# Performance work log

Hardware: AMD Instinct MI355X
Metric: run time of the kernel (lower is better)

Reference implementation:

```python
import jax, jax.numpy as jnp
import numpy as np

NUM_FEAT = 1024
NUM_GROUP = 16
DIM_K = NUM_FEAT // NUM_GROUP  # 64
FEAT_DIM = 64
WAVE_LENGTH = 1000.0


def position_embedding(box, ctx_box):
    # box: (M,4), ctx_box: (N,4) corner encoding -> (M*N, 64)
    xmin, ymin, xmax, ymax = jnp.split(box, 4, axis=1)            # (M,1) each
    bw = xmax - xmin + 1.0
    bh = ymax - ymin + 1.0
    cx = 0.5 * (xmin + xmax)
    cy = 0.5 * (ymin + ymax)
    cxmin, cymin, cxmax, cymax = jnp.split(ctx_box, 4, axis=1)    # (N,1) each
    cbw = cxmax - cxmin + 1.0
    cbh = cymax - cymin + 1.0
    ccx = 0.5 * (cxmin + cxmax)
    ccy = 0.5 * (cymin + cymax)
    dx = jnp.log(jnp.clip(jnp.abs((cx - ccx.T) / bw), 1e-3))      # (M,N)
    dy = jnp.log(jnp.clip(jnp.abs((cy - ccy.T) / bh), 1e-3))
    dw = jnp.log(cbw.T / bw)
    dh = jnp.log(cbh.T / bh)
    pos = jnp.stack((dx, dy, dw, dh), axis=2)                     # (M,N,4)
    feat_range = jnp.arange(FEAT_DIM // 8, dtype=jnp.float32)     # (8,)
    dim_mat = jnp.power(jnp.float32(WAVE_LENGTH), (8.0 / FEAT_DIM) * feat_range)
    div = (100.0 * pos)[..., None] / dim_mat                      # (M,N,4,8)
    emb = jnp.concatenate((jnp.sin(div), jnp.cos(div)), axis=3)   # (M,N,4,16)
    M, N = pos.shape[0], pos.shape[1]
    return emb.reshape(M * N, FEAT_DIM)


def setup_inputs() -> dict:
    key = jax.random.key(0)
    ks = jax.random.split(key, 12)
    M, N = 512, 1024

    def make_boxes(k, n):
        k1, k2 = jax.random.split(k)
        xy = jax.random.uniform(k1, (n, 2), dtype=jnp.float32) * 800.0
        wh = jax.random.uniform(k2, (n, 2), dtype=jnp.float32) * 200.0 + 1.0
        return jnp.concatenate([xy, xy + wh], axis=1)             # valid corners

    return {
        "feat": jax.random.normal(ks[0], (M, NUM_FEAT), dtype=jnp.float32),
        "ctx_feat": jax.random.normal(ks[1], (N, NUM_FEAT), dtype=jnp.float32),
        "box": make_boxes(ks[2], M),
        "ctx_box": make_boxes(ks[3], N),
        # torch Linear stores weight as (out, in); apply as x @ W.T + b
        "w_fc_gt": jax.random.normal(ks[4], (NUM_FEAT, 1024), dtype=jnp.float32) * 0.01,
        "b_fc_gt": jnp.zeros((NUM_FEAT,), dtype=jnp.float32),
        "w_fc_ctx": jax.random.normal(ks[5], (NUM_FEAT, 1024), dtype=jnp.float32) * 0.01,
        "b_fc_ctx": jnp.zeros((NUM_FEAT,), dtype=jnp.float32),
        "w_pos_gt": jax.random.normal(ks[6], (NUM_GROUP, FEAT_DIM), dtype=jnp.float32) * 0.01,
        "b_pos_gt": jnp.zeros((NUM_GROUP,), dtype=jnp.float32),
        "w_pos_ctx": jax.random.normal(ks[7], (NUM_GROUP, FEAT_DIM), dtype=jnp.float32) * 0.01,
        "b_pos_ctx": jnp.zeros((NUM_GROUP,), dtype=jnp.float32),
        # grouped 1x1 conv (16384 -> 1024, groups=16): per-group weight (64 out, 1024 in)
        "w_conv": jax.random.normal(ks[8], (NUM_GROUP, DIM_K, NUM_FEAT), dtype=jnp.float32) * 0.02,
        "b_conv": jnp.zeros((NUM_FEAT,), dtype=jnp.float32),
    }


def reference(feat, ctx_feat, box, ctx_box,
              w_fc_gt, b_fc_gt, w_fc_ctx, b_fc_ctx,
              w_pos_gt, b_pos_gt, w_pos_ctx, b_pos_ctx,
              w_conv, b_conv):
    M, N = feat.shape[0], ctx_feat.shape[0]
    # positional bias per group: (M*N,64) -relu-> linear -> (G,M,N)
    pe_gt = jax.nn.relu(position_embedding(box, ctx_box))
    pos_gt = (pe_gt @ w_pos_gt.T + b_pos_gt).T.reshape(NUM_GROUP, M, N)
    pe_ctx = jax.nn.relu(position_embedding(ctx_box, box))
    pos_ctx = (pe_ctx @ w_pos_ctx.T + b_pos_ctx).T.reshape(NUM_GROUP, N, M)
    # grouped projections
    q = (feat @ w_fc_gt.T + b_fc_gt).reshape(M, NUM_GROUP, DIM_K)
    k = (ctx_feat @ w_fc_ctx.T + b_fc_ctx).reshape(N, NUM_GROUP, DIM_K)
    scores = jnp.einsum('mgd,ngd->gmn', q, k) / np.float32(np.sqrt(DIM_K))  # (G,M,N)
    # gt <- ctx attention with log-position bias
    w1 = jax.nn.softmax(jnp.log(jnp.clip(pos_gt, 1e-6)) + scores, axis=-1)  # (G,M,N)
    att1 = jnp.einsum('gmn,nc->mgc', w1, ctx_feat)                          # (M,G,1024)
    out_gt = jnp.einsum('mgc,goc->mgo', att1, w_conv).reshape(M, NUM_FEAT) + b_conv
    # ctx <- gt attention (note: original module reuses gt_ctx_linear_out here)
    w2 = jax.nn.softmax(jnp.log(jnp.clip(pos_ctx, 1e-6)) + scores.transpose(0, 2, 1), axis=-1)  # (G,N,M)
    att2 = jnp.einsum('gnm,mc->ngc', w2, feat)                              # (N,G,1024)
    out_ctx = jnp.einsum('ngc,goc->ngo', att2, w_conv).reshape(N, NUM_FEAT) + b_conv
    return out_gt, out_ctx
```

## Files before the change

kernel.cpp:

```cpp
#include <hip/hip_runtime.h>
#include <math.h>


typedef __attribute__((ext_vector_type(8))) short short8;
typedef __attribute__((ext_vector_type(4))) float floatx4;
typedef __attribute__((ext_vector_type(4))) _Float16 half4;
typedef __attribute__((ext_vector_type(4))) unsigned uint4v;

__device__ inline unsigned short f32_bf16_rne(float x) {
    union { float f; unsigned u; } v; v.f = x;
    unsigned u = v.u;
    return (unsigned short)((u + 0x7fffu + ((u >> 16) & 1u)) >> 16);
}

__device__ inline unsigned fbits(float x) {
    union { float f; unsigned u; } v; v.f = x; return v.u;
}
__device__ inline float bitsf(unsigned u) {
    union { unsigned u; float f; } v; v.u = u; return v.f;
}

__device__ __forceinline__ floatx4 mfma16(short8 a, short8 b, floatx4 c) {
    return __builtin_amdgcn_mfma_f32_16x16x32_bf16(a, b, c, 0, 0, 0);
}

__device__ __forceinline__ void gemm_tile_pack(
    const unsigned short* __restrict__ Ab, int lda,
    const unsigned short* __restrict__ Bb, int ldb, int K,
    unsigned short* __restrict__ out_base,
    const float* __restrict__ biasvec,
    unsigned short* As, unsigned short* Bs)
{
    const int tid = threadIdx.x;
    const int lr = tid >> 3;
    const int lk = (tid & 7) * 8;
    const int lane = tid & 63;
    const int wave = tid >> 6;
    const int qr = (wave >> 1) * 32;
    const int qc = (wave & 1) * 32;
    const int m = lane & 15;
    const int quad = lane >> 4;

    const unsigned short* Ap  = Ab + (long long)lr * lda + lk;
    const unsigned short* Ap2 = Ap + 32LL * lda;
    const unsigned short* Bp  = Bb + (long long)lr * ldb + lk;
    const unsigned short* Bp2 = Bp + 32LL * ldb;
    unsigned short* AsW  = As + lr * 72 + lk;
    unsigned short* AsW2 = As + (lr + 32) * 72 + lk;
    unsigned short* BsW  = Bs + lr * 72 + lk;
    unsigned short* BsW2 = Bs + (lr + 32) * 72 + lk;
    const unsigned short* a0p = As + (qr + m) * 72 + quad * 8;
    const unsigned short* b0p = Bs + (qc + m) * 72 + quad * 8;

    floatx4 acc00 = {0.f,0.f,0.f,0.f}, acc01 = {0.f,0.f,0.f,0.f};
    floatx4 acc10 = {0.f,0.f,0.f,0.f}, acc11 = {0.f,0.f,0.f,0.f};

    int4 pa0 = *(const int4*)Ap;
    int4 pa1 = *(const int4*)Ap2;
    int4 pb0 = *(const int4*)Bp;
    int4 pb1 = *(const int4*)Bp2;
    int4 qa0 = *(const int4*)(Ap + 64);
    int4 qa1 = *(const int4*)(Ap2 + 64);
    int4 qb0 = *(const int4*)(Bp + 64);
    int4 qb1 = *(const int4*)(Bp2 + 64);

    for (int k0 = 0; ; ) {
        __syncthreads();
        *(int4*)AsW  = pa0;
        *(int4*)AsW2 = pa1;
        *(int4*)BsW  = pb0;
        *(int4*)BsW2 = pb1;
        __syncthreads();
        pa0 = qa0; pa1 = qa1; pb0 = qb0; pb1 = qb1;
        const int kf = k0 + 128;
        if (kf < K) {
            qa0 = *(const int4*)(Ap + kf);
            qa1 = *(const int4*)(Ap2 + kf);
            qb0 = *(const int4*)(Bp + kf);
            qb1 = *(const int4*)(Bp2 + kf);
        }
        #pragma unroll
        for (int kk = 0; kk < 64; kk += 32) {
            short8 a0 = *(const short8*)(a0p + kk);
            short8 a1 = *(const short8*)(a0p + 16 * 72 + kk);
            short8 b0 = *(const short8*)(b0p + kk);
            short8 b1 = *(const short8*)(b0p + 16 * 72 + kk);
            acc00 = mfma16(a0, b0, acc00);
            acc01 = mfma16(a0, b1, acc01);
            acc10 = mfma16(a1, b0, acc10);
            acc11 = mfma16(a1, b1, acc11);
        }
        k0 += 64;
        if (k0 >= K) break;
    }

    float bias0 = 0.f, bias1 = 0.f;
    if (biasvec) { bias0 = biasvec[qc + m]; bias1 = biasvec[qc + 16 + m]; }

    __syncthreads();
    const floatx4 accs[2][2] = { {acc00, acc01}, {acc10, acc11} };
    #pragma unroll
    for (int i = 0; i < 2; ++i)
        #pragma unroll
        for (int r = 0; r < 4; ++r) {
            const int lrow = qr + i * 16 + quad * 4 + r;
            #pragma unroll
            for (int j = 0; j < 2; ++j) {
                const int lcol = qc + j * 16 + m;
                float val = accs[i][j][r] + (j ? bias1 : bias0);
                As[lrow * 72 + lcol] = f32_bf16_rne(val);
            }
        }
    __syncthreads();
    #pragma unroll
    for (int h = 0; h < 2; ++h) {
        const int f = h * 2048 + tid * 8;
        const int lanep = (f >> 3) & 63;
        const int part = (f >> 9) & 1;
        const int ploc = f >> 10;
        const int row = ploc * 16 + (lanep & 15);
        const int col = part * 32 + ((lanep >> 4) << 3);
        short8 v8 = *(const short8*)&As[row * 72 + col];
        *(short8*)(out_base + f) = v8;
    }
}

__global__ __launch_bounds__(256) void cast_kernel(
    const float* __restrict__ s0, unsigned short* __restrict__ d0,
    const float* __restrict__ s1, unsigned short* __restrict__ d1,
    const float* __restrict__ s2, unsigned short* __restrict__ d2,
    const float* __restrict__ s3, unsigned short* __restrict__ d3,
    const float* __restrict__ s4, unsigned short* __restrict__ d4)
{
    int bc = blockIdx.x;
    const float* s; unsigned short* d;
    if (bc < 512)       { s = s0; d = d0; }
    else if (bc < 1536) { s = s1; d = d1; bc -= 512; }
    else if (bc < 2560) { s = s2; d = d2; bc -= 1536; }
    else if (bc < 3584) { s = s3; d = d3; bc -= 2560; }
    else                { s = s4; d = d4; bc -= 3584; }
    const int idx = (bc * 256 + threadIdx.x) * 4;
    float4 v = *(const float4*)(s + idx);
    ushort4 o;
    o.x = f32_bf16_rne(v.x); o.y = f32_bf16_rne(v.y);
    o.z = f32_bf16_rne(v.z); o.w = f32_bf16_rne(v.w);
    *(ushort4*)(d + idx) = o;
}

__global__ __launch_bounds__(256) void posproj_kernel(
    const float* __restrict__ box, const float* __restrict__ ctx_box,
    const float* __restrict__ w_gt, const float* __restrict__ b_gt,
    const float* __restrict__ w_ctx, const float* __restrict__ b_ctx,
    _Float16* __restrict__ bias_gt, _Float16* __restrict__ bias_ctx,
    const unsigned short* __restrict__ in_bf, const unsigned short* __restrict__ wgt,
    const unsigned short* __restrict__ wctx,
    const float* __restrict__ bgt, const float* __restrict__ bctx,
    unsigned short* __restrict__ qk_pack,
    const unsigned short* __restrict__ wconv, unsigned short* __restrict__ vt_pack)
{
    __shared__ __align__(16) unsigned short smem[64 * 72 * 2];
    const int i = blockIdx.x;

    if (i < 4608 && (i % 6) == 0) {
        const int gi = i / 6;
        const int z = gi / 384;
        const int rem = gi - z * 384;
        const int g = rem / 24;
        const int cc = rem - g * 24;
        unsigned short* As = smem;
        unsigned short* Bs = smem + 64 * 72;
        if (z == 0) {
            const int bm = cc * 64;
            const unsigned short* B = (bm < 512) ? wgt : wctx;
            const float* bias = (bm < 512) ? bgt : bctx;
            gemm_tile_pack(in_bf + (long long)bm * 1024, 1024,
                           B + (long long)g * 65536, 1024, 1024,
                           qk_pack + ((long long)g * 96 + cc * 4) * 1024,
                           bias + g * 64, As, Bs);
        } else {
            gemm_tile_pack(wconv + (long long)g * 65536, 1024,
                           in_bf + (long long)cc * 65536, 1024, 1024,
                           vt_pack + ((long long)g * 24 + cc) * 4096,
                           nullptr, As, Bs);
        }
        return;
    }

    const int pi = (i < 4608) ? (i - i / 6 - 1) : (i - 768);
    const bool first = (pi < 2048);
    const long long blk = first ? pi : (pi - 2048);
    const float* boxA = first ? box : ctx_box;
    const float* boxB = first ? ctx_box : box;
    const float* w_pos = first ? w_gt : w_ctx;
    const float* b_pos = first ? b_gt : b_ctx;
    _Float16* out = first ? bias_gt : bias_ctx;
    const int shift = first ? 10 : 9;

    unsigned short* BsH = smem;
    unsigned short* BsL = smem + 16 * 72;
    float* posL = (float*)(smem + 32 * 72);
    _Float16* stg = (_Float16*)(posL + 4 * 68);

    const int tid = threadIdx.x;

    {
        const int g = tid >> 4;
        const int d = (tid & 15) * 4;
        float4 wv = *(const float4*)(w_pos + g * 64 + d);
        unsigned u0 = fbits(wv.x), u1 = fbits(wv.y);
        unsigned u2 = fbits(wv.z), u3 = fbits(wv.w);
        unsigned r0 = fbits(wv.x - bitsf(u0 & 0xFFFF0000u));
        unsigned r1 = fbits(wv.y - bitsf(u1 & 0xFFFF0000u));
        unsigned r2 = fbits(wv.z - bitsf(u2 & 0xFFFF0000u));
        unsigned r3 = fbits(wv.w - bitsf(u3 & 0xFFFF0000u));
        uint2 hv, lv;
        hv.x = (u0 >> 16) | (u1 & 0xFFFF0000u);
        hv.y = (u2 >> 16) | (u3 & 0xFFFF0000u);
        lv.x = (r0 >> 16) | (r1 & 0xFFFF0000u);
        lv.y = (r2 >> 16) | (r3 & 0xFFFF0000u);
        *(uint2*)&BsH[g * 72 + d] = hv;
        *(uint2*)&BsL[g * 72 + d] = lv;
    }
    __syncthreads();

    const int lane = tid & 63;
    const int w = tid >> 6;
    const int m = lane & 15;
    const int quad = lane >> 4;
    const bool qlow = (quad < 2);
    const float phase = (quad & 1) ? 1.57079632679f : 0.0f;
    const float bpv = b_pos[m];

    const unsigned short* bpH = &BsH[m * 72 + quad * 8];
    const unsigned short* bpL = &BsL[m * 72 + quad * 8];
    short8 bH0 = *(const short8*)bpH;
    short8 bH1 = *(const short8*)(bpH + 32);
    short8 bL0 = *(const short8*)bpL;
    short8 bL1 = *(const short8*)(bpL + 32);

    const float w100[8] = {100.f, 42.169650342f, 17.782794100f, 7.498942093f,
                           3.162277660f, 1.333521432f, 0.562341325f, 0.237137371f};
    const long long pbase = blk * 256;

    for (int it = 0; it < 4; ++it) {
        const long long pb = pbase + it * 64;

        {
            const int pl = tid & 63;
            const int p = tid >> 6;
            const long long pair = pb + pl;
            const int i2 = (int)(pair >> shift);
            const int j2 = (int)(pair & ((1 << shift) - 1));
            float4 ba = *(const float4*)(boxA + i2 * 4);
            float4 bb = *(const float4*)(boxB + j2 * 4);
            float posv;
            if (p == 0) {
                float r = __builtin_amdgcn_rcpf(ba.z - ba.x + 1.f);
                posv = __logf(fmaxf(fabsf((0.5f*(ba.x+ba.z) - 0.5f*(bb.x+bb.z)) * r), 1e-3f));
            } else if (p == 1) {
                float r = __builtin_amdgcn_rcpf(ba.w - ba.y + 1.f);
                posv = __logf(fmaxf(fabsf((0.5f*(ba.y+ba.w) - 0.5f*(bb.y+bb.w)) * r), 1e-3f));
            } else if (p == 2) {
                float r = __builtin_amdgcn_rcpf(ba.z - ba.x + 1.f);
                posv = __logf((bb.z - bb.x + 1.f) * r);
            } else {
                float r = __builtin_amdgcn_rcpf(ba.w - ba.y + 1.f);
                posv = __logf((bb.w - bb.y + 1.f) * r);
            }
            posL[p * 68 + pl] = posv;
        }
        __syncthreads();

        const int plB = w * 16 + m;
        const float pos_lo = posL[(qlow ? 0 : 1) * 68 + plB];
        const float pos_hi = posL[(qlow ? 2 : 3) * 68 + plB];

        unsigned hp0[4], lp0[4], hp1[4], lp1[4];
        #pragma unroll
        for (int fi = 0; fi < 4; ++fi) {
            float x0 = fmaxf(__sinf(fmaf(w100[2*fi],     pos_lo, phase)), 0.f);
            float x1 = fmaxf(__sinf(fmaf(w100[2*fi + 1], pos_lo, phase)), 0.f);
            unsigned u0 = fbits(x0), u1 = fbits(x1);
            unsigned r0 = fbits(x0 - bitsf(u0 & 0xFFFF0000u));
            unsigned r1 = fbits(x1 - bitsf(u1 & 0xFFFF0000u));
            hp0[fi] = (u0 >> 16) | (u1 & 0xFFFF0000u);
            lp0[fi] = (r0 >> 16) | (r1 & 0xFFFF0000u);
            float y0 = fmaxf(__sinf(fmaf(w100[2*fi],     pos_hi, phase)), 0.f);
            float y1 = fmaxf(__sinf(fmaf(w100[2*fi + 1], pos_hi, phase)), 0.f);
            unsigned v0 = fbits(y0), v1 = fbits(y1);
            unsigned s0r = fbits(y0 - bitsf(v0 & 0xFFFF0000u));
            unsigned s1r = fbits(y1 - bitsf(v1 & 0xFFFF0000u));
            hp1[fi] = (v0 >> 16) | (v1 & 0xFFFF0000u);
            lp1[fi] = (s0r >> 16) | (s1r & 0xFFFF0000u);
        }
        union { uint4v u; short8 s; } cH0, cL0, cH1, cL1;
        cH0.u = (uint4v){hp0[0], hp0[1], hp0[2], hp0[3]};
        cL0.u = (uint4v){lp0[0], lp0[1], lp0[2], lp0[3]};
        cH1.u = (uint4v){hp1[0], hp1[1], hp1[2], hp1[3]};
        cL1.u = (uint4v){lp1[0], lp1[1], lp1[2], lp1[3]};

        floatx4 acc = {0.f, 0.f, 0.f, 0.f};
        acc = mfma16(cH0.s, bH0, acc);
        acc = mfma16(cH1.s, bH1, acc);
        acc = mfma16(cH0.s, bL0, acc);
        acc = mfma16(cH1.s, bL1, acc);
        acc = mfma16(cL0.s, bH0, acc);
        acc = mfma16(cL1.s, bH1, acc);

        #pragma unroll
        for (int r = 0; r < 4; ++r)
            stg[m * 68 + w * 16 + quad * 4 + r] =
                (_Float16)__logf(fmaxf(acc[r] + bpv, 1e-6f));
        __syncthreads();

        const int g2 = tid >> 4, c16 = tid & 15;
        *(half4*)(out + (long long)g2 * 524288 + pb + c16 * 4) =
            *(const half4*)&stg[g2 * 68 + c16 * 4];
    }
}

template <int NC>
__device__ __forceinline__ void attn_body(
    int g, int bx,
    const unsigned short* __restrict__ qk, int pA, int pB0,
    const _Float16* __restrict__ bias,
    const unsigned short* __restrict__ vt, int cc0,
    const float* __restrict__ b_conv, float* __restrict__ outp,
    unsigned short* wpack, float* redA, float* redB)
{
    constexpr int NCOL = NC * 64;
    constexpr int WS = NCOL + 8;
    constexpr int SHIFT = (NC == 16) ? 10 : 9;

    const int bm = bx * 16;
    const int tid = threadIdx.x;
    const int lane = tid & 63;
    const int w = tid >> 6;
    const int m = lane & 15;
    const int quad = lane >> 4;

    _Float16* bb = (_Float16*)wpack;
    {
        const _Float16* bsrc = bias + (long long)g * 524288 + (long long)bm * NCOL;
        #pragma unroll
        for (int i = 0; i < (16 * NCOL) / (256 * 8); ++i) {
            const int idx = (i * 256 + tid) * 8;
            const int row = idx >> SHIFT;
            const int col = idx & (NCOL - 1);
            *(int4*)(bb + row * WS + col) = *(const int4*)(bsrc + idx);
        }
    }

    const unsigned short* abase = qk + ((long long)(g * 96 + pA)) * 1024;
    short8 aq0 = *(const short8*)(abase + lane * 8);
    short8 aq1 = *(const short8*)(abase + 512 + lane * 8);

    const unsigned short* bptr = qk + ((long long)(g * 96 + pB0 + w)) * 1024 + lane * 8;
    short8 B0[2], B1[2];
    B0[0] = *(const short8*)bptr;
    B1[0] = *(const short8*)(bptr + 512);
    B0[1] = *(const short8*)(bptr + 4096);
    B1[1] = *(const short8*)(bptr + 4096 + 512);

    __syncthreads();

    const _Float16* brow = bb + (quad * 4) * WS + w * 16 + m;

    float v[NC][4];
    #pragma unroll
    for (int c = 0; c < NC; ++c) {
        float bv[4];
        #pragma unroll
        for (int r = 0; r < 4; ++r)
            bv[r] = (float)brow[r * WS + c * 64];
        floatx4 acc = {0.f, 0.f, 0.f, 0.f};
        acc = mfma16(aq0, B0[c & 1], acc);
        acc = mfma16(aq1, B1[c & 1], acc);
        if (c + 2 < NC) {
            const unsigned short* nb = bptr + (long long)(c + 2) * 4096;
            B0[c & 1] = *(const short8*)nb;
            B1[c & 1] = *(const short8*)(nb + 512);
        }
        #pragma unroll
        for (int r = 0; r < 4; ++r)
            v[c][r] = fmaf(0.125f, acc[r], bv[r]);
    }

    const unsigned short* vptr = vt + ((long long)(g * 24 + cc0)) * 4096
                               + w * 1024 + lane * 8;
    short8 V0[2], V1[2];
    V0[0] = *(const short8*)vptr;
    V1[0] = *(const short8*)(vptr + 512);
    V0[1] = *(const short8*)(vptr + 4096);
    V1[1] = *(const short8*)(vptr + 4096 + 512);

    float rmax[4];
    #pragma unroll
    for (int r = 0; r < 4; ++r) {
        float mx = v[0][r];
        #pragma unroll
        for (int c = 1; c < NC; ++c) mx = fmaxf(mx, v[c][r]);
        #pragma unroll
        for (int off = 1; off < 16; off <<= 1)
            mx = fmaxf(mx, __shfl_xor(mx, off, 64));
        rmax[r] = mx;
    }
    if (m == 0) {
        #pragma unroll
        for (int r = 0; r < 4; ++r) redA[w * 16 + quad * 4 + r] = rmax[r];
    }
    __syncthreads();
    #pragma unroll
    for (int r = 0; r < 4; ++r)
        rmax[r] = fmaxf(fmaxf(redA[quad*4+r], redA[16 + quad*4+r]),
                        fmaxf(redA[32 + quad*4+r], redA[48 + quad*4+r]));

    float rsum[4] = {0.f, 0.f, 0.f, 0.f};
    #pragma unroll
    for (int c = 0; c < NC; ++c)
        #pragma unroll
        for (int r = 0; r < 4; ++r) {
            v[c][r] = __expf(v[c][r] - rmax[r]);
            rsum[r] += v[c][r];
        }
    #pragma unroll
    for (int r = 0; r < 4; ++r)
        #pragma unroll
        for (int off = 1; off < 16; off <<= 1)
            rsum[r] += __shfl_xor(rsum[r], off, 64);
    if (m == 0) {
        #pragma unroll
        for (int r = 0; r < 4; ++r) redB[w * 16 + quad * 4 + r] = rsum[r];
    }
    __syncthreads();
    float rinv[4];
    #pragma unroll
    for (int r = 0; r < 4; ++r)
        rinv[r] = 1.f / (redB[quad*4+r] + redB[16 + quad*4+r] +
                         redB[32 + quad*4+r] + redB[48 + quad*4+r]);

    #pragma unroll
    for (int c = 0; c < NC; ++c)
        #pragma unroll
        for (int r = 0; r < 4; ++r)
            wpack[(quad * 4 + r) * WS + c * 64 + w * 16 + m] =
                f32_bf16_rne(v[c][r] * rinv[r]);

    __syncthreads();

    floatx4 oacc = {0.f, 0.f, 0.f, 0.f};
    const unsigned short* awp = wpack + m * WS + quad * 8;
    #pragma unroll
    for (int kc = 0; kc < NC; ++kc) {
        short8 a0 = *(const short8*)(awp + kc * 64);
        short8 a1 = *(const short8*)(awp + kc * 64 + 32);
        oacc = mfma16(a0, V0[kc & 1], oacc);
        oacc = mfma16(a1, V1[kc & 1], oacc);
        if (kc + 2 < NC) {
            const unsigned short* nv = vptr + (long long)(kc + 2) * 4096;
            V0[kc & 1] = *(const short8*)nv;
            V1[kc & 1] = *(const short8*)(nv + 512);
        }
    }

    const int o = w * 16 + m;
    const float bc = b_conv[g * 64 + o];
    __syncthreads();
    float* ot = (float*)wpack;
    #pragma unroll
    for (int r = 0; r < 4; ++r)
        ot[(quad * 4 + r) * 68 + o] = oacc[r] + bc;
    __syncthreads();
    const int orow = tid >> 4, oc4 = (tid & 15) * 4;
    float4 ov = *(const float4*)&ot[orow * 68 + oc4];
    *(float4*)(outp + (long long)(bm + orow) * 1024 + g * 64 + oc4) = ov;
}

__global__ __launch_bounds__(256) void attn_out_kernel(
    const unsigned short* __restrict__ qk_pack,
    const _Float16* __restrict__ bias_gt, const _Float16* __restrict__ bias_ctx,
    const unsigned short* __restrict__ vt_pack, const float* __restrict__ b_conv,
    float* __restrict__ out_gt, float* __restrict__ out_ctx)
{
    __shared__ __align__(16) unsigned short wpack[16 * 1032];
    __shared__ float redA[64], redB[64];

    const int bx = blockIdx.x;
    if (bx < 512) {
        const int rb = bx & 31;
        attn_body<16>(bx >> 5, rb, qk_pack, rb, 32,
                      bias_gt, vt_pack, 8, b_conv, out_gt,
                      wpack, redA, redB);
    } else {
        const int b2 = bx - 512;
        const int rb = b2 & 63;
        attn_body<8>(b2 >> 6, rb, qk_pack, 32 + rb, 0,
                     bias_ctx, vt_pack, 0, b_conv, out_ctx,
                     wpack, redA, redB);
    }
}

extern "C" void kernel_launch(void* const* d_in, const int* in_sizes, int n_in,
                              void* d_out, int out_size, void* d_ws, size_t ws_size,
                              hipStream_t stream)
{
    const float* feat     = (const float*)d_in[0];
    const float* ctx_feat = (const float*)d_in[1];
    const float* box      = (const float*)d_in[2];
    const float* ctx_box  = (const float*)d_in[3];
    const float* w_fc_gt  = (const float*)d_in[4];
    const float* b_fc_gt  = (const float*)d_in[5];
    const float* w_fc_ctx = (const float*)d_in[6];
    const float* b_fc_ctx = (const float*)d_in[7];
    const float* w_pos_gt = (const float*)d_in[8];
    const float* b_pos_gt = (const float*)d_in[9];
    const float* w_pos_ctx= (const float*)d_in[10];
    const float* b_pos_ctx= (const float*)d_in[11];
    const float* w_conv   = (const float*)d_in[12];
    const float* b_conv   = (const float*)d_in[13];

    float* ws = (float*)d_ws;
    unsigned short* in_bf   = (unsigned short*)ws;
    unsigned short* ctx_bf  = in_bf + 524288LL;
    unsigned short* qk_pack = in_bf + 1572864LL;
    _Float16* bias_gt  = (_Float16*)(ws + 1572864LL);
    _Float16* bias_ctx = (_Float16*)(ws + 5767168LL);
    unsigned short* wconv_bf = (unsigned short*)(ws + 9961472LL);
    unsigned short* vt_pack  = (unsigned short*)(ws + 10485760LL);
    unsigned short* wfcgt_bf = (unsigned short*)(ws + 11272192LL);
    unsigned short* wfcctx_bf= wfcgt_bf + 1048576LL;

    float* out_gt  = (float*)d_out;
    float* out_ctx = (float*)d_out + 524288LL;

    hipLaunchKernelGGL(cast_kernel, dim3(4608), dim3(256), 0, stream,
                       feat, in_bf,
                       ctx_feat, ctx_bf,
                       w_fc_gt, wfcgt_bf,
                       w_fc_ctx, wfcctx_bf,
                       w_conv, wconv_bf);

    hipLaunchKernelGGL(posproj_kernel, dim3(4864), dim3(256), 0, stream,
                       box, ctx_box, w_pos_gt, b_pos_gt, w_pos_ctx, b_pos_ctx,
                       bias_gt, bias_ctx,
                       in_bf, wfcgt_bf, wfcctx_bf, b_fc_gt, b_fc_ctx, qk_pack,
                       wconv_bf, vt_pack);

    hipLaunchKernelGGL(attn_out_kernel, dim3(1536), dim3(256), 0, stream,
                       qk_pack, bias_gt, bias_ctx, vt_pack, b_conv, out_gt, out_ctx);
}
```

Before: 150.9 us.

## Load GEMM MFMA operands directly from global memory, bypassing LDS staging

The projection GEMM tile no longer stages A and B tiles through shared memory with two barriers per k-step. Each wave now loads its MFMA operand fragments directly from global memory into registers, prefetching one k-step ahead. Shared memory for the fused kernel is halved, which may help occupancy of the position-projection blocks. The cost is that each operand row is fetched redundantly by several waves, and the per-lane 16-byte global loads are less coalesced, so more traffic goes to the cache.

```diff
diff --git a/kernel.cpp b/kernel.cpp
--- a/kernel.cpp
+++ b/kernel.cpp
@@ -24,16 +24,14 @@
     return __builtin_amdgcn_mfma_f32_16x16x32_bf16(a, b, c, 0, 0, 0);
 }
 
-__device__ __forceinline__ void gemm_tile_pack(
+__device__ __forceinline__ void gemm_tile_pack_direct(
     const unsigned short* __restrict__ Ab, int lda,
     const unsigned short* __restrict__ Bb, int ldb, int K,
     unsigned short* __restrict__ out_base,
     const float* __restrict__ biasvec,
-    unsigned short* As, unsigned short* Bs)
+    unsigned short* As)
 {
     const int tid = threadIdx.x;
-    const int lr = tid >> 3;
-    const int lk = (tid & 7) * 8;
     const int lane = tid & 63;
     const int wave = tid >> 6;
     const int qr = (wave >> 1) * 32;
@@ -41,63 +39,53 @@
     const int m = lane & 15;
     const int quad = lane >> 4;
 
-    const unsigned short* Ap  = Ab + (long long)lr * lda + lk;
-    const unsigned short* Ap2 = Ap + 32LL * lda;
-    const unsigned short* Bp  = Bb + (long long)lr * ldb + lk;
-    const unsigned short* Bp2 = Bp + 32LL * ldb;
-    unsigned short* AsW  = As + lr * 72 + lk;
-    unsigned short* AsW2 = As + (lr + 32) * 72 + lk;
-    unsigned short* BsW  = Bs + lr * 72 + lk;
-    unsigned short* BsW2 = Bs + (lr + 32) * 72 + lk;
-    const unsigned short* a0p = As + (qr + m) * 72 + quad * 8;
-    const unsigned short* b0p = Bs + (qc + m) * 72 + quad * 8;
+    const unsigned short* Arow0 = Ab + (long long)(qr + m) * lda + quad * 8;
+    const unsigned short* Arow1 = Arow0 + 16LL * lda;
+    const unsigned short* Brow0 = Bb + (long long)(qc + m) * ldb + quad * 8;
+    const unsigned short* Brow1 = Brow0 + 16LL * ldb;
 
     floatx4 acc00 = {0.f,0.f,0.f,0.f}, acc01 = {0.f,0.f,0.f,0.f};
     floatx4 acc10 = {0.f,0.f,0.f,0.f}, acc11 = {0.f,0.f,0.f,0.f};
 
-    int4 pa0 = *(const int4*)Ap;
-    int4 pa1 = *(const int4*)Ap2;
-    int4 pb0 = *(const int4*)Bp;
-    int4 pb1 = *(const int4*)Bp2;
-    int4 qa0 = *(const int4*)(Ap + 64);
-    int4 qa1 = *(const int4*)(Ap2 + 64);
-    int4 qb0 = *(const int4*)(Bp + 64);
-    int4 qb1 = *(const int4*)(Bp2 + 64);
+    short8 ca0 = *(const short8*)(Arow0);
+    short8 ca1 = *(const short8*)(Arow1);
+    short8 cb0 = *(const short8*)(Brow0);
+    short8 cb1 = *(const short8*)(Brow1);
+    short8 da0 = *(const short8*)(Arow0 + 32);
+    short8 da1 = *(const short8*)(Arow1 + 32);
+    short8 db0 = *(const short8*)(Brow0 + 32);
+    short8 db1 = *(const short8*)(Brow1 + 32);
 
     for (int k0 = 0; ; ) {
-        __syncthreads();
-        *(int4*)AsW  = pa0;
-        *(int4*)AsW2 = pa1;
-        *(int4*)BsW  = pb0;
-        *(int4*)BsW2 = pb1;
-        __syncthreads();
-        pa0 = qa0; pa1 = qa1; pb0 = qb0; pb1 = qb1;
-        const int kf = k0 + 128;
+        const int kf = k0 + 64;
+        short8 ea0, ea1, eb0, eb1, fa0, fa1, fb0, fb1;
         if (kf < K) {
-            qa0 = *(const int4*)(Ap + kf);
-            qa1 = *(const int4*)(Ap2 + kf);
-            qb0 = *(const int4*)(Bp + kf);
-            qb1 = *(const int4*)(Bp2 + kf);
-        }
-        #pragma unroll
-        for (int kk = 0; kk < 64; kk += 32) {
-            short8 a0 = *(const short8*)(a0p + kk);
-            short8 a1 = *(const short8*)(a0p + 16 * 72 + kk);
-            short8 b0 = *(const short8*)(b0p + kk);
-            short8 b1 = *(const short8*)(b0p + 16 * 72 + kk);
-            acc00 = mfma16(a0, b0, acc00);
-            acc01 = mfma16(a0, b1, acc01);
-            acc10 = mfma16(a1, b0, acc10);
-            acc11 = mfma16(a1, b1, acc11);
-        }
-        k0 += 64;
+            ea0 = *(const short8*)(Arow0 + kf);
+            ea1 = *(const short8*)(Arow1 + kf);
+            eb0 = *(const short8*)(Brow0 + kf);
+            eb1 = *(const short8*)(Brow1 + kf);
+            fa0 = *(const short8*)(Arow0 + kf + 32);
+            fa1 = *(const short8*)(Arow1 + kf + 32);
+            fb0 = *(const short8*)(Brow0 + kf + 32);
+            fb1 = *(const short8*)(Brow1 + kf + 32);
+        }
+        acc00 = mfma16(ca0, cb0, acc00);
+        acc01 = mfma16(ca0, cb1, acc01);
+        acc10 = mfma16(ca1, cb0, acc10);
+        acc11 = mfma16(ca1, cb1, acc11);
+        acc00 = mfma16(da0, db0, acc00);
+        acc01 = mfma16(da0, db1, acc01);
+        acc10 = mfma16(da1, db0, acc10);
+        acc11 = mfma16(da1, db1, acc11);
+        k0 = kf;
         if (k0 >= K) break;
+        ca0 = ea0; ca1 = ea1; cb0 = eb0; cb1 = eb1;
+        da0 = fa0; da1 = fa1; db0 = fb0; db1 = fb1;
     }
 
     float bias0 = 0.f, bias1 = 0.f;
     if (biasvec) { bias0 = biasvec[qc + m]; bias1 = biasvec[qc + 16 + m]; }
 
-    __syncthreads();
     const floatx4 accs[2][2] = { {acc00, acc01}, {acc10, acc11} };
     #pragma unroll
     for (int i = 0; i < 2; ++i)
@@ -158,7 +146,7 @@
     unsigned short* __restrict__ qk_pack,
     const unsigned short* __restrict__ wconv, unsigned short* __restrict__ vt_pack)
 {
-    __shared__ __align__(16) unsigned short smem[64 * 72 * 2];
+    __shared__ __align__(16) unsigned short smem[64 * 72];
     const int i = blockIdx.x;
 
     if (i < 4608 && (i % 6) == 0) {
@@ -167,21 +155,19 @@
         const int rem = gi - z * 384;
         const int g = rem / 24;
         const int cc = rem - g * 24;
-        unsigned short* As = smem;
-        unsigned short* Bs = smem + 64 * 72;
         if (z == 0) {
             const int bm = cc * 64;
             const unsigned short* B = (bm < 512) ? wgt : wctx;
             const float* bias = (bm < 512) ? bgt : bctx;
-            gemm_tile_pack(in_bf + (long long)bm * 1024, 1024,
-                           B + (long long)g * 65536, 1024, 1024,
-                           qk_pack + ((long long)g * 96 + cc * 4) * 1024,
-                           bias + g * 64, As, Bs);
+            gemm_tile_pack_direct(in_bf + (long long)bm * 1024, 1024,
+                                  B + (long long)g * 65536, 1024, 1024,
+                                  qk_pack + ((long long)g * 96 + cc * 4) * 1024,
+                                  bias + g * 64, smem);
         } else {
-            gemm_tile_pack(wconv + (long long)g * 65536, 1024,
-                           in_bf + (long long)cc * 65536, 1024, 1024,
-                           vt_pack + ((long long)g * 24 + cc) * 4096,
-                           nullptr, As, Bs);
+            gemm_tile_pack_direct(wconv + (long long)g * 65536, 1024,
+                                  in_bf + (long long)cc * 65536, 1024, 1024,
+                                  vt_pack + ((long long)g * 24 + cc) * 4096,
+                                  nullptr, smem);
         }
         return;
     }
```

After: 228.7 us. 51.6% more time.

## Fold log-position bias into softmax as multiplier, drop max pass, defer normalization

Applied to the files above, without the earlier changes.

The position-bias kernel now stores the clipped bias itself instead of its log, and the attention softmax computes exp(score/8)*bias directly. This rests on the identity exp(log p + s) = p*exp(s). The row-max reduction and its barrier are removed, and the unnormalized weights are written in place into shared memory. The 1/sum scaling is applied after the PV matmul, which drops another full pass over the weights and a sync. Without max subtraction the exponentials are no longer guarded against overflow, so correctness depends on the scores staying bounded.

```diff
diff --git a/kernel.cpp b/kernel.cpp
--- a/kernel.cpp
+++ b/kernel.cpp
@@ -18,6 +18,9 @@
 }
 __device__ inline float bitsf(unsigned u) {
     union { unsigned u; float f; } v; v.u = u; return v.f;
+}
+__device__ inline float h16f(unsigned short u) {
+    union { unsigned short u; _Float16 h; } v; v.u = u; return (float)v.h;
 }
 
 __device__ __forceinline__ floatx4 mfma16(short8 a, short8 b, floatx4 c) {
@@ -310,7 +313,7 @@
         #pragma unroll
         for (int r = 0; r < 4; ++r)
             stg[m * 68 + w * 16 + quad * 4 + r] =
-                (_Float16)__logf(fmaxf(acc[r] + bpv, 1e-6f));
+                (_Float16)fmaxf(acc[r] + bpv, 1e-6f);
         __syncthreads();
 
         const int g2 = tid >> 4, c16 = tid & 15;
@@ -326,7 +329,7 @@
     const _Float16* __restrict__ bias,
     const unsigned short* __restrict__ vt, int cc0,
     const float* __restrict__ b_conv, float* __restrict__ outp,
-    unsigned short* wpack, float* redA, float* redB)
+    unsigned short* wpack, float* redB)
 {
     constexpr int NCOL = NC * 64;
     constexpr int WS = NCOL + 8;
@@ -339,9 +342,9 @@
     const int m = lane & 15;
     const int quad = lane >> 4;
 
-    _Float16* bb = (_Float16*)wpack;
     {
         const _Float16* bsrc = bias + (long long)g * 524288 + (long long)bm * NCOL;
+        _Float16* bb = (_Float16*)wpack;
         #pragma unroll
         for (int i = 0; i < (16 * NCOL) / (256 * 8); ++i) {
             const int idx = (i * 256 + tid) * 8;
@@ -364,15 +367,9 @@
 
     __syncthreads();
 
-    const _Float16* brow = bb + (quad * 4) * WS + w * 16 + m;
-
     float v[NC][4];
     #pragma unroll
     for (int c = 0; c < NC; ++c) {
-        float bv[4];
-        #pragma unroll
-        for (int r = 0; r < 4; ++r)
-            bv[r] = (float)brow[r * WS + c * 64];
         floatx4 acc = {0.f, 0.f, 0.f, 0.f};
         acc = mfma16(aq0, B0[c & 1], acc);
         acc = mfma16(aq1, B1[c & 1], acc);
@@ -383,7 +380,7 @@
         }
         #pragma unroll
         for (int r = 0; r < 4; ++r)
-            v[c][r] = fmaf(0.125f, acc[r], bv[r]);
+            v[c][r] = acc[r];
     }
 
     const unsigned short* vptr = vt + ((long long)(g * 24 + cc0)) * 4096
@@ -394,34 +391,17 @@
     V0[1] = *(const short8*)(vptr + 4096);
     V1[1] = *(const short8*)(vptr + 4096 + 512);
 
-    float rmax[4];
-    #pragma unroll
-    for (int r = 0; r < 4; ++r) {
-        float mx = v[0][r];
-        #pragma unroll
-        for (int c = 1; c < NC; ++c) mx = fmaxf(mx, v[c][r]);
-        #pragma unroll
-        for (int off = 1; off < 16; off <<= 1)
-            mx = fmaxf(mx, __shfl_xor(mx, off, 64));
-        rmax[r] = mx;
-    }
-    if (m == 0) {
-        #pragma unroll
-        for (int r = 0; r < 4; ++r) redA[w * 16 + quad * 4 + r] = rmax[r];
-    }
-    __syncthreads();
-    #pragma unroll
-    for (int r = 0; r < 4; ++r)
-        rmax[r] = fmaxf(fmaxf(redA[quad*4+r], redA[16 + quad*4+r]),
-                        fmaxf(redA[32 + quad*4+r], redA[48 + quad*4+r]));
-
+    const int slot0 = (quad * 4) * WS + w * 16 + m;
     float rsum[4] = {0.f, 0.f, 0.f, 0.f};
     #pragma unroll
     for (int c = 0; c < NC; ++c)
         #pragma unroll
         for (int r = 0; r < 4; ++r) {
-            v[c][r] = __expf(v[c][r] - rmax[r]);
-            rsum[r] += v[c][r];
+            const int a = slot0 + r * WS + c * 64;
+            float p = h16f(wpack[a]);
+            float e = exp2f(v[c][r] * 0.18033688f) * p;
+            rsum[r] += e;
+            wpack[a] = f32_bf16_rne(e);
         }
     #pragma unroll
     for (int r = 0; r < 4; ++r)
@@ -433,20 +413,12 @@
         for (int r = 0; r < 4; ++r) redB[w * 16 + quad * 4 + r] = rsum[r];
     }
     __syncthreads();
+
     float rinv[4];
     #pragma unroll
     for (int r = 0; r < 4; ++r)
         rinv[r] = 1.f / (redB[quad*4+r] + redB[16 + quad*4+r] +
                          redB[32 + quad*4+r] + redB[48 + quad*4+r]);
-
-    #pragma unroll
-    for (int c = 0; c < NC; ++c)
-        #pragma unroll
-        for (int r = 0; r < 4; ++r)
-            wpack[(quad * 4 + r) * WS + c * 64 + w * 16 + m] =
-                f32_bf16_rne(v[c][r] * rinv[r]);
-
-    __syncthreads();
 
     floatx4 oacc = {0.f, 0.f, 0.f, 0.f};
     const unsigned short* awp = wpack + m * WS + quad * 8;
@@ -469,7 +441,7 @@
     float* ot = (float*)wpack;
     #pragma unroll
     for (int r = 0; r < 4; ++r)
-        ot[(quad * 4 + r) * 68 + o] = oacc[r] + bc;
+        ot[(quad * 4 + r) * 68 + o] = fmaf(oacc[r], rinv[r], bc);
     __syncthreads();
     const int orow = tid >> 4, oc4 = (tid & 15) * 4;
     float4 ov = *(const float4*)&ot[orow * 68 + oc4];
@@ -483,20 +455,20 @@
     float* __restrict__ out_gt, float* __restrict__ out_ctx)
 {
     __shared__ __align__(16) unsigned short wpack[16 * 1032];
-    __shared__ float redA[64], redB[64];
+    __shared__ float redB[64];
 
     const int bx = blockIdx.x;
     if (bx < 512) {
         const int rb = bx & 31;
         attn_body<16>(bx >> 5, rb, qk_pack, rb, 32,
                       bias_gt, vt_pack, 8, b_conv, out_gt,
-                      wpack, redA, redB);
+                      wpack, redB);
     } else {
         const int b2 = bx - 512;
         const int rb = b2 & 63;
         attn_body<8>(b2 >> 6, rb, qk_pack, 32 + rb, 0,
                      bias_ctx, vt_pack, 0, b_conv, out_ctx,
-                     wpack, redA, redB);
+                     wpack, redB);
     }
 }
 
```

New measurement: 148.6 us. About the same (-1.5%).
